# Performance work log

Measured on AMD Instinct MI355X. Metric: run time of the kernel, lower is better.

## Reference

```python
import jax, jax.numpy as jnp
import numpy as np
from jax.scipy.linalg import solve_triangular

B, D, O, K, R, HID = 8192, 64, 32, 15, 3, 60
LOG_2PI = float(np.log(2.0 * np.pi))


def setup_inputs() -> dict:
    key = jax.random.key(0)
    ks = jax.random.split(key, 12)
    state_mean = jax.random.normal(ks[0], (B, D), jnp.float32)
    A = jax.random.normal(ks[1], (B, D, D), jnp.float32) * 0.1
    state_cov = jnp.einsum('bik,bjk->bij', A, A) / D + 0.5 * jnp.eye(D, dtype=jnp.float32)
    obs = jax.random.normal(ks[2], (B, O), jnp.float32)
    w1 = jax.random.normal(ks[3], (HID, D), jnp.float32) / np.sqrt(D)
    b1 = jnp.zeros((HID,), jnp.float32)
    w2 = jax.random.normal(ks[4], (K, HID), jnp.float32) / np.sqrt(HID)
    b2 = jnp.zeros((K,), jnp.float32)
    basis = jax.random.normal(ks[5], (K, D, D), jnp.float32) * 0.01
    pnf = jax.random.normal(ks[6], (D, R), jnp.float32) * 0.1
    pnd = jnp.ones((D,), jnp.float32) * 0.1
    onf = jax.random.normal(ks[7], (O, R), jnp.float32) * 0.1
    ond = jnp.ones((O,), jnp.float32) * 0.1
    Hw = jax.random.normal(ks[8], (O, D), jnp.float32) / np.sqrt(D)
    Hb = jnp.zeros((O,), jnp.float32)
    return dict(state_mean=state_mean, state_cov=state_cov, obs=obs,
                w1=w1, b1=b1, w2=w2, b2=b2, basis=basis,
                pnf=pnf, pnd=pnd, onf=onf, ond=ond, Hw=Hw, Hb=Hb)


def _rkn_cell(state_mean, state_cov, obs, w1, b1, w2, b2, basis, pnf, pnd, onf, ond, Hw, Hb):
    # ---- predict step: locally linear dynamics ----
    h = jax.nn.elu(state_mean @ w1.T + b1)
    weights = jax.nn.softmax(h @ w2.T + b2, axis=-1)          # [B, K]
    F = jnp.einsum('bn,nij->bij', weights, basis)             # [B, D, D]
    pred_mean = jnp.einsum('bij,bj->bi', F, state_mean)
    FPFT = jnp.einsum('bij,bjk,blk->bil', F, state_cov, F)
    Q = pnf @ pnf.T + jnp.diag(jnp.exp(pnd))                  # [D, D] process noise
    pred_cov = FPFT + Q[None]

    # ---- update step ----
    obs_pred = pred_mean @ Hw.T + Hb
    innovation = obs - obs_pred                               # [B, O]
    HPH = jnp.einsum('oi,bij,pj->bop', Hw, pred_cov, Hw)      # [B, O, O]
    Rn = onf @ onf.T + jnp.diag(jnp.exp(ond))                 # [O, O] obs noise
    S = HPH + Rn[None]                                        # innovation cov
    PHt = jnp.einsum('bij,oj->bio', pred_cov, Hw)             # [B, D, O]

    L = jnp.linalg.cholesky(S)                                # [B, O, O]
    eyeO = jnp.broadcast_to(jnp.eye(O, dtype=S.dtype), (S.shape[0], O, O))
    Linv = solve_triangular(L, eyeO, lower=True)              # L^{-1}
    S_inv = jnp.einsum('bko,bkp->bop', Linv, Linv)            # cholesky_inverse

    Kg = jnp.einsum('bio,bop->bip', PHt, S_inv)               # Kalman gain [B, D, O]
    post_mean = pred_mean + jnp.einsum('bio,bo->bi', Kg, innovation)
    KH = jnp.einsum('bio,oj->bij', Kg, Hw)
    post_cov = jnp.einsum('bij,bjk->bik', jnp.eye(D, dtype=KH.dtype)[None] - KH, pred_cov)

    log_det = 2.0 * jnp.sum(jnp.log(jnp.diagonal(L, axis1=-2, axis2=-1)), axis=-1)
    quad = jnp.einsum('bo,bop,bp->b', innovation, S_inv, innovation)
    log_likelihood = -0.5 * (log_det + quad + O * LOG_2PI)
    return post_mean, post_cov, log_likelihood


def reference(state_mean, state_cov, obs, w1, b1, w2, b2, basis, pnf, pnd, onf, ond, Hw, Hb):
    return _rkn_cell(state_mean, state_cov, obs, w1, b1, w2, b2, basis, pnf, pnd, onf, ond, Hw, Hb)
```

## Files before the change

### kernel.cpp

```cpp
#include <hip/hip_runtime.h>
#include <math.h>

#define NB   8192
#define DD   64
#define OO   32
#define KK   15
#define HID  60

#define LDF  68
#define LDT  72
#define SST  36
#define XOFF (32*LDF)

#define LOG2PI 1.8378770664093453f

__global__ __launch_bounds__(256, 2)
void rkn_kernel(const float* __restrict__ state_mean,
                const float* __restrict__ state_cov,
                const float* __restrict__ obs,
                const float* __restrict__ w1,
                const float* __restrict__ b1,
                const float* __restrict__ w2,
                const float* __restrict__ b2,
                const float* __restrict__ basis,
                const float* __restrict__ pnf,
                const float* __restrict__ pnd,
                const float* __restrict__ onf,
                const float* __restrict__ ond,
                const float* __restrict__ Hw,
                const float* __restrict__ Hb,
                float* __restrict__ out_pm,
                float* __restrict__ out_pc,
                float* __restrict__ out_ll)
{
  __shared__ __align__(16) float sF [64*LDF];
  __shared__ __align__(16) float sP [64*LDF];
  __shared__ __align__(16) float sT [64*LDT];
  __shared__ __align__(16) float sHw[32*LDF];
  __shared__ __align__(16) float sS [32*SST];
  __shared__ __align__(16) float sm_[64];
  __shared__ __align__(16) float pm_[64];
  __shared__ __align__(16) float h_ [64];
  __shared__ __align__(16) float inn_[32];
  __shared__ __align__(16) float y_ [32];
  __shared__ float wts_[16];
  __shared__ float redA[32];
  __shared__ float rdiag_[32];
  __shared__ float qd_;
  __shared__ __align__(16) float spnf[64*4];
  __shared__ float spd[64];
  __shared__ __align__(16) float sonf[32*4];
  __shared__ float sod[32];

  const int t = threadIdx.x;
  const int b = blockIdx.x;

  {
    const float4* cov4 = (const float4*)(state_cov + (size_t)b * 4096);
    #pragma unroll
    for (int r = 0; r < 4; r++) {
      int idx = t + 256*r;
      int row = idx >> 4, c4 = idx & 15;
      *(float4*)&sP[row*LDF + c4*4] = cov4[idx];
    }
    const float4* hw4 = (const float4*)Hw;
    #pragma unroll
    for (int r = 0; r < 2; r++) {
      int idx = t + 256*r;
      int row = idx >> 4, c4 = idx & 15;
      *(float4*)&sHw[row*LDF + c4*4] = hw4[idx];
    }
    if (t < 64) {
      sm_[t] = state_mean[(size_t)b*64 + t];
      spnf[t*4+0] = pnf[t*3+0];
      spnf[t*4+1] = pnf[t*3+1];
      spnf[t*4+2] = pnf[t*3+2];
      spnf[t*4+3] = 0.0f;
      spd[t] = expf(pnd[t]);
    }
    if (t < 32) {
      sonf[t*4+0] = onf[t*3+0];
      sonf[t*4+1] = onf[t*3+1];
      sonf[t*4+2] = onf[t*3+2];
      sonf[t*4+3] = 0.0f;
      sod[t] = expf(ond[t]);
    }
  }
  __syncthreads();

  if (t < HID) {
    const float4* w1r = (const float4*)(w1 + t*64);
    float acc = 0.0f;
    #pragma unroll
    for (int m = 0; m < 16; m++) {
      float4 wv = w1r[m];
      float4 sv = *(const float4*)&sm_[4*m];
      acc += wv.x*sv.x + wv.y*sv.y + wv.z*sv.z + wv.w*sv.w;
    }
    acc += b1[t];
    h_[t] = (acc > 0.0f) ? acc : expm1f(acc);
  }
  __syncthreads();

  if (t < KK) {
    const float* w2r = w2 + t*60;
    float acc = 0.0f;
    for (int m = 0; m < 60; m++) acc += w2r[m]*h_[m];
    wts_[t] = acc + b2[t];
  }
  __syncthreads();

  if (t == 0) {
    float mx = wts_[0];
    for (int k = 1; k < KK; k++) mx = fmaxf(mx, wts_[k]);
    float s = 0.0f;
    for (int k = 0; k < KK; k++) { float e = expf(wts_[k]-mx); wts_[k] = e; s += e; }
    float inv = 1.0f/s;
    for (int k = 0; k < KK; k++) wts_[k] *= inv;
  }
  __syncthreads();

  {
    float w[KK];
    #pragma unroll
    for (int k = 0; k < KK; k++) w[k] = wts_[k];
    const float4* bas4 = (const float4*)basis;
    #pragma unroll
    for (int r = 0; r < 4; r++) {
      int idx = t + 256*r;
      float4 acc; acc.x = 0; acc.y = 0; acc.z = 0; acc.w = 0;
      #pragma unroll
      for (int k = 0; k < KK; k++) {
        float4 bv = bas4[k*1024 + idx];
        acc.x += w[k]*bv.x; acc.y += w[k]*bv.y;
        acc.z += w[k]*bv.z; acc.w += w[k]*bv.w;
      }
      int row = idx >> 4, c4 = idx & 15;
      *(float4*)&sF[row*LDF + c4*4] = acc;
    }
  }
  __syncthreads();

  const int tr = t >> 4, tc = t & 15;
  const int i0 = tr*4, j0 = tc*4;

  {
    float acc[4][4] = {};
    for (int k = 0; k < 64; k += 4) {
      float4 a[4], bb[4];
      #pragma unroll
      for (int r = 0; r < 4; r++) a[r] = *(const float4*)&sF[(i0+r)*LDF + k];
      #pragma unroll
      for (int kk = 0; kk < 4; kk++) bb[kk] = *(const float4*)&sP[(k+kk)*LDF + j0];
      #pragma unroll
      for (int r = 0; r < 4; r++) {
        float4 av = a[r];
        acc[r][0] += av.x*bb[0].x + av.y*bb[1].x + av.z*bb[2].x + av.w*bb[3].x;
        acc[r][1] += av.x*bb[0].y + av.y*bb[1].y + av.z*bb[2].y + av.w*bb[3].y;
        acc[r][2] += av.x*bb[0].z + av.y*bb[1].z + av.z*bb[2].z + av.w*bb[3].z;
        acc[r][3] += av.x*bb[0].w + av.y*bb[1].w + av.z*bb[2].w + av.w*bb[3].w;
      }
    }
    #pragma unroll
    for (int r = 0; r < 4; r++) {
      float4 st; st.x = acc[r][0]; st.y = acc[r][1]; st.z = acc[r][2]; st.w = acc[r][3];
      *(float4*)&sT[(i0+r)*LDT + j0] = st;
    }
  }
  if (t < 64) {
    float acc = 0.0f;
    #pragma unroll
    for (int m = 0; m < 16; m++) {
      float4 fv = *(const float4*)&sF[t*LDF + 4*m];
      float4 sv = *(const float4*)&sm_[4*m];
      acc += fv.x*sv.x + fv.y*sv.y + fv.z*sv.z + fv.w*sv.w;
    }
    pm_[t] = acc;
  }
  __syncthreads();

  {
    float acc[4][4] = {};
    for (int k = 0; k < 64; k += 4) {
      float4 a[4], bb[4];
      #pragma unroll
      for (int r = 0; r < 4; r++) a[r] = *(const float4*)&sT[(i0+r)*LDT + k];
      #pragma unroll
      for (int c = 0; c < 4; c++) bb[c] = *(const float4*)&sF[(j0+c)*LDF + k];
      #pragma unroll
      for (int r = 0; r < 4; r++) {
        #pragma unroll
        for (int c = 0; c < 4; c++) {
          acc[r][c] += a[r].x*bb[c].x + a[r].y*bb[c].y + a[r].z*bb[c].z + a[r].w*bb[c].w;
        }
      }
    }
    #pragma unroll
    for (int r = 0; r < 4; r++) {
      int i = i0 + r;
      float4 st;
      float* pst = (float*)&st;
      #pragma unroll
      for (int c = 0; c < 4; c++) {
        int j = j0 + c;
        float q = spnf[i*4+0]*spnf[j*4+0] + spnf[i*4+1]*spnf[j*4+1] + spnf[i*4+2]*spnf[j*4+2];
        if (i == j) q += spd[i];
        pst[c] = acc[r][c] + q;
      }
      *(float4*)&sP[i*LDF + j0] = st;
    }
  }
  if (t < 32) {
    float acc = 0.0f;
    #pragma unroll
    for (int m = 0; m < 16; m++) {
      float4 hv = *(const float4*)&sHw[t*LDF + 4*m];
      float4 pv = *(const float4*)&pm_[4*m];
      acc += hv.x*pv.x + hv.y*pv.y + hv.z*pv.z + hv.w*pv.w;
    }
    inn_[t] = obs[(size_t)b*32 + t] - (acc + Hb[t]);
  }
  __syncthreads();

  {
    const int hr0 = (t >> 4)*2, hc0 = (t & 15)*4;
    float acc[2][4] = {};
    for (int k = 0; k < 64; k += 4) {
      float4 a0 = *(const float4*)&sHw[hr0*LDF + k];
      float4 a1 = *(const float4*)&sHw[(hr0+1)*LDF + k];
      float4 bb[4];
      #pragma unroll
      for (int kk = 0; kk < 4; kk++) bb[kk] = *(const float4*)&sP[(k+kk)*LDF + hc0];
      #pragma unroll
      for (int c = 0; c < 4; c++) {
        float* pb0 = (float*)&bb[0]; float* pb1 = (float*)&bb[1];
        float* pb2 = (float*)&bb[2]; float* pb3 = (float*)&bb[3];
        acc[0][c] += a0.x*pb0[c] + a0.y*pb1[c] + a0.z*pb2[c] + a0.w*pb3[c];
        acc[1][c] += a1.x*pb0[c] + a1.y*pb1[c] + a1.z*pb2[c] + a1.w*pb3[c];
      }
    }
    float4 s0, s1;
    s0.x = acc[0][0]; s0.y = acc[0][1]; s0.z = acc[0][2]; s0.w = acc[0][3];
    s1.x = acc[1][0]; s1.y = acc[1][1]; s1.z = acc[1][2]; s1.w = acc[1][3];
    *(float4*)&sT[hr0*LDF + hc0] = s0;
    *(float4*)&sT[(hr0+1)*LDF + hc0] = s1;
  }
  __syncthreads();

  const int so = t >> 3, sp0 = (t & 7)*4;

  {
    float acc[4] = {};
    for (int k = 0; k < 64; k += 4) {
      float4 av = *(const float4*)&sT[so*LDF + k];
      #pragma unroll
      for (int c = 0; c < 4; c++) {
        float4 bv = *(const float4*)&sHw[(sp0+c)*LDF + k];
        acc[c] += av.x*bv.x + av.y*bv.y + av.z*bv.z + av.w*bv.w;
      }
    }
    #pragma unroll
    for (int c = 0; c < 4; c++) {
      int p = sp0 + c;
      float rn = sonf[so*4+0]*sonf[p*4+0] + sonf[so*4+1]*sonf[p*4+1] + sonf[so*4+2]*sonf[p*4+2];
      if (so == p) rn += sod[so];
      sS[so*SST + p] = acc[c] + rn;
    }
  }
  __syncthreads();

  for (int k = 0; k < 32; k++) {
    float dk  = sS[k*SST + k];
    float cik = sS[so*SST + k];
    float cj[4];
    #pragma unroll
    for (int c = 0; c < 4; c++) cj[c] = sS[(sp0+c)*SST + k];
    __syncthreads();
    float rd = 1.0f/dk;
    #pragma unroll
    for (int c = 0; c < 4; c++) {
      int j = sp0 + c;
      if (so > k && j > k) sS[so*SST + j] -= cik*cj[c]*rd;
    }
    if (k >= sp0 && k < sp0+4) {
      float sd = sqrtf(dk);
      if (so > k)       sS[so*SST + k] = cik/sd;
      else if (so == k) sS[k*SST + k]  = sd;
    }
    __syncthreads();
  }

  if (t < 32) {
    float d = sS[t*SST + t];
    rdiag_[t] = 1.0f/d;
    redA[t]  = logf(d);
  }
  __syncthreads();

  if (t < 65) {
    float x[32];
    if (t < 64) {
      #pragma unroll
      for (int i = 0; i < 32; i++) x[i] = sT[i*LDF + t];
    } else {
      #pragma unroll
      for (int i = 0; i < 32; i++) x[i] = inn_[i];
    }
    #pragma unroll
    for (int m = 0; m < 32; m++) {
      x[m] *= rdiag_[m];
      #pragma unroll
      for (int i = m+1; i < 32; i++) x[i] -= sS[i*SST + m] * x[m];
    }
    if (t < 64) {
      #pragma unroll
      for (int i = 0; i < 32; i++) sT[XOFF + i*LDF + t] = x[i];
    } else {
      float q = 0.0f;
      #pragma unroll
      for (int i = 0; i < 32; i++) { y_[i] = x[i]; q += x[i]*x[i]; }
      qd_ = q;
    }
  }
  __syncthreads();

  {
    float acc[4][4] = {};
    for (int o = 0; o < 32; o += 2) {
      float4 xa0 = *(const float4*)&sT[XOFF + o*LDF + i0];
      float4 xb0 = *(const float4*)&sT[XOFF + o*LDF + j0];
      float4 xa1 = *(const float4*)&sT[XOFF + (o+1)*LDF + i0];
      float4 xb1 = *(const float4*)&sT[XOFF + (o+1)*LDF + j0];
      const float* a0 = (const float*)&xa0; const float* b0 = (const float*)&xb0;
      const float* a1 = (const float*)&xa1; const float* b1p = (const float*)&xb1;
      #pragma unroll
      for (int r = 0; r < 4; r++) {
        #pragma unroll
        for (int c = 0; c < 4; c++) {
          acc[r][c] += a0[r]*b0[c] + a1[r]*b1p[c];
        }
      }
    }
    #pragma unroll
    for (int r = 0; r < 4; r++) {
      int i = i0 + r;
      float4 st;
      st.x = sP[i*LDF + j0+0] - acc[r][0];
      st.y = sP[i*LDF + j0+1] - acc[r][1];
      st.z = sP[i*LDF + j0+2] - acc[r][2];
      st.w = sP[i*LDF + j0+3] - acc[r][3];
      *(float4*)&out_pc[(size_t)b*4096 + i*64 + j0] = st;
    }
  }
  if (t < 64) {
    float acc = pm_[t];
    #pragma unroll
    for (int i = 0; i < 32; i++) acc += sT[XOFF + i*LDF + t] * y_[i];
    out_pm[(size_t)b*64 + t] = acc;
  }
  if (t == 0) {
    float ld = 0.0f;
    for (int k = 0; k < 32; k++) ld += redA[k];
    out_ll[b] = -0.5f*(2.0f*ld + qd_ + 32.0f*LOG2PI);
  }
}

extern "C" void kernel_launch(void* const* d_in, const int* in_sizes, int n_in,
                              void* d_out, int out_size, void* d_ws, size_t ws_size,
                              hipStream_t stream) {
  const float* state_mean = (const float*)d_in[0];
  const float* state_cov  = (const float*)d_in[1];
  const float* obs        = (const float*)d_in[2];
  const float* w1         = (const float*)d_in[3];
  const float* b1         = (const float*)d_in[4];
  const float* w2         = (const float*)d_in[5];
  const float* b2         = (const float*)d_in[6];
  const float* basis      = (const float*)d_in[7];
  const float* pnf        = (const float*)d_in[8];
  const float* pnd        = (const float*)d_in[9];
  const float* onf        = (const float*)d_in[10];
  const float* ond        = (const float*)d_in[11];
  const float* Hw         = (const float*)d_in[12];
  const float* Hb         = (const float*)d_in[13];

  const int Bn = in_sizes[0] / 64;
  float* out = (float*)d_out;
  float* out_pm = out;
  float* out_pc = out + (size_t)Bn*64;
  float* out_ll = out + (size_t)Bn*64 + (size_t)Bn*4096;

  hipLaunchKernelGGL(rkn_kernel, dim3(Bn), dim3(256), 0, stream,
                     state_mean, state_cov, obs, w1, b1, w2, b2, basis,
                     pnf, pnd, onf, ond, Hw, Hb, out_pm, out_pc, out_ll);
}
```

Measured before the change: 2.736 ms.

## Double block size, shrink per-thread tiles, warp-level Cholesky via shuffles

```diff
diff --git a/kernel.cpp b/kernel.cpp
--- a/kernel.cpp
+++ b/kernel.cpp
@@ -14,7 +14,9 @@
 
 #define LOG2PI 1.8378770664093453f
 
-__global__ __launch_bounds__(256, 2)
+typedef float f32x4 __attribute__((ext_vector_type(4)));
+
+__global__ __launch_bounds__(512, 4)
 void rkn_kernel(const float* __restrict__ state_mean,
                 const float* __restrict__ state_cov,
                 const float* __restrict__ obs,
@@ -58,17 +60,15 @@
   {
     const float4* cov4 = (const float4*)(state_cov + (size_t)b * 4096);
     #pragma unroll
-    for (int r = 0; r < 4; r++) {
-      int idx = t + 256*r;
+    for (int r = 0; r < 2; r++) {
+      int idx = t + 512*r;
       int row = idx >> 4, c4 = idx & 15;
       *(float4*)&sP[row*LDF + c4*4] = cov4[idx];
     }
     const float4* hw4 = (const float4*)Hw;
-    #pragma unroll
-    for (int r = 0; r < 2; r++) {
-      int idx = t + 256*r;
-      int row = idx >> 4, c4 = idx & 15;
-      *(float4*)&sHw[row*LDF + c4*4] = hw4[idx];
+    {
+      int row = t >> 4, c4 = t & 15;
+      *(float4*)&sHw[row*LDF + c4*4] = hw4[t];
     }
     if (t < 64) {
       sm_[t] = state_mean[(size_t)b*64 + t];
@@ -126,8 +126,8 @@
     for (int k = 0; k < KK; k++) w[k] = wts_[k];
     const float4* bas4 = (const float4*)basis;
     #pragma unroll
-    for (int r = 0; r < 4; r++) {
-      int idx = t + 256*r;
+    for (int r = 0; r < 2; r++) {
+      int idx = t + 512*r;
       float4 acc; acc.x = 0; acc.y = 0; acc.z = 0; acc.w = 0;
       #pragma unroll
       for (int k = 0; k < KK; k++) {
@@ -142,27 +142,26 @@
   __syncthreads();
 
   const int tr = t >> 4, tc = t & 15;
-  const int i0 = tr*4, j0 = tc*4;
-
-  {
-    float acc[4][4] = {};
+  const int i0 = tr*2, j0 = tc*4;
+
+  {
+    float acc[2][4] = {};
     for (int k = 0; k < 64; k += 4) {
-      float4 a[4], bb[4];
-      #pragma unroll
-      for (int r = 0; r < 4; r++) a[r] = *(const float4*)&sF[(i0+r)*LDF + k];
+      float4 a0 = *(const float4*)&sF[(i0  )*LDF + k];
+      float4 a1 = *(const float4*)&sF[(i0+1)*LDF + k];
+      float4 bb[4];
       #pragma unroll
       for (int kk = 0; kk < 4; kk++) bb[kk] = *(const float4*)&sP[(k+kk)*LDF + j0];
-      #pragma unroll
-      for (int r = 0; r < 4; r++) {
-        float4 av = a[r];
-        acc[r][0] += av.x*bb[0].x + av.y*bb[1].x + av.z*bb[2].x + av.w*bb[3].x;
-        acc[r][1] += av.x*bb[0].y + av.y*bb[1].y + av.z*bb[2].y + av.w*bb[3].y;
-        acc[r][2] += av.x*bb[0].z + av.y*bb[1].z + av.z*bb[2].z + av.w*bb[3].z;
-        acc[r][3] += av.x*bb[0].w + av.y*bb[1].w + av.z*bb[2].w + av.w*bb[3].w;
-      }
-    }
-    #pragma unroll
-    for (int r = 0; r < 4; r++) {
+      const float* b0 = (const float*)&bb[0]; const float* b1p = (const float*)&bb[1];
+      const float* b2p = (const float*)&bb[2]; const float* b3 = (const float*)&bb[3];
+      #pragma unroll
+      for (int c = 0; c < 4; c++) {
+        acc[0][c] += a0.x*b0[c] + a0.y*b1p[c] + a0.z*b2p[c] + a0.w*b3[c];
+        acc[1][c] += a1.x*b0[c] + a1.y*b1p[c] + a1.z*b2p[c] + a1.w*b3[c];
+      }
+    }
+    #pragma unroll
+    for (int r = 0; r < 2; r++) {
       float4 st; st.x = acc[r][0]; st.y = acc[r][1]; st.z = acc[r][2]; st.w = acc[r][3];
       *(float4*)&sT[(i0+r)*LDT + j0] = st;
     }
@@ -180,23 +179,19 @@
   __syncthreads();
 
   {
-    float acc[4][4] = {};
+    float acc[2][4] = {};
     for (int k = 0; k < 64; k += 4) {
-      float4 a[4], bb[4];
-      #pragma unroll
-      for (int r = 0; r < 4; r++) a[r] = *(const float4*)&sT[(i0+r)*LDT + k];
-      #pragma unroll
-      for (int c = 0; c < 4; c++) bb[c] = *(const float4*)&sF[(j0+c)*LDF + k];
-      #pragma unroll
-      for (int r = 0; r < 4; r++) {
-        #pragma unroll
-        for (int c = 0; c < 4; c++) {
-          acc[r][c] += a[r].x*bb[c].x + a[r].y*bb[c].y + a[r].z*bb[c].z + a[r].w*bb[c].w;
-        }
-      }
-    }
-    #pragma unroll
-    for (int r = 0; r < 4; r++) {
+      float4 a0 = *(const float4*)&sT[(i0  )*LDT + k];
+      float4 a1 = *(const float4*)&sT[(i0+1)*LDT + k];
+      #pragma unroll
+      for (int c = 0; c < 4; c++) {
+        float4 bv = *(const float4*)&sF[(j0+c)*LDF + k];
+        acc[0][c] += a0.x*bv.x + a0.y*bv.y + a0.z*bv.z + a0.w*bv.w;
+        acc[1][c] += a1.x*bv.x + a1.y*bv.y + a1.z*bv.z + a1.w*bv.w;
+      }
+    }
+    #pragma unroll
+    for (int r = 0; r < 2; r++) {
       int i = i0 + r;
       float4 st;
       float* pst = (float*)&st;
@@ -223,33 +218,26 @@
   __syncthreads();
 
   {
-    const int hr0 = (t >> 4)*2, hc0 = (t & 15)*4;
-    float acc[2][4] = {};
+    const int hr = t >> 4, hc0 = (t & 15)*4;
+    float acc[4] = {};
     for (int k = 0; k < 64; k += 4) {
-      float4 a0 = *(const float4*)&sHw[hr0*LDF + k];
-      float4 a1 = *(const float4*)&sHw[(hr0+1)*LDF + k];
+      float4 a = *(const float4*)&sHw[hr*LDF + k];
       float4 bb[4];
       #pragma unroll
       for (int kk = 0; kk < 4; kk++) bb[kk] = *(const float4*)&sP[(k+kk)*LDF + hc0];
-      #pragma unroll
-      for (int c = 0; c < 4; c++) {
-        float* pb0 = (float*)&bb[0]; float* pb1 = (float*)&bb[1];
-        float* pb2 = (float*)&bb[2]; float* pb3 = (float*)&bb[3];
-        acc[0][c] += a0.x*pb0[c] + a0.y*pb1[c] + a0.z*pb2[c] + a0.w*pb3[c];
-        acc[1][c] += a1.x*pb0[c] + a1.y*pb1[c] + a1.z*pb2[c] + a1.w*pb3[c];
-      }
-    }
-    float4 s0, s1;
-    s0.x = acc[0][0]; s0.y = acc[0][1]; s0.z = acc[0][2]; s0.w = acc[0][3];
-    s1.x = acc[1][0]; s1.y = acc[1][1]; s1.z = acc[1][2]; s1.w = acc[1][3];
-    *(float4*)&sT[hr0*LDF + hc0] = s0;
-    *(float4*)&sT[(hr0+1)*LDF + hc0] = s1;
-  }
-  __syncthreads();
-
-  const int so = t >> 3, sp0 = (t & 7)*4;
-
-  {
+      const float* b0 = (const float*)&bb[0]; const float* b1p = (const float*)&bb[1];
+      const float* b2p = (const float*)&bb[2]; const float* b3 = (const float*)&bb[3];
+      #pragma unroll
+      for (int c = 0; c < 4; c++)
+        acc[c] += a.x*b0[c] + a.y*b1p[c] + a.z*b2p[c] + a.w*b3[c];
+    }
+    float4 s0; s0.x = acc[0]; s0.y = acc[1]; s0.z = acc[2]; s0.w = acc[3];
+    *(float4*)&sT[hr*LDF + hc0] = s0;
+  }
+  __syncthreads();
+
+  if (t < 256) {
+    const int so = t >> 3, sp0 = (t & 7)*4;
     float acc[4] = {};
     for (int k = 0; k < 64; k += 4) {
       float4 av = *(const float4*)&sT[so*LDF + k];
@@ -269,35 +257,36 @@
   }
   __syncthreads();
 
-  for (int k = 0; k < 32; k++) {
-    float dk  = sS[k*SST + k];
-    float cik = sS[so*SST + k];
-    float cj[4];
-    #pragma unroll
-    for (int c = 0; c < 4; c++) cj[c] = sS[(sp0+c)*SST + k];
-    __syncthreads();
-    float rd = 1.0f/dk;
-    #pragma unroll
-    for (int c = 0; c < 4; c++) {
-      int j = sp0 + c;
-      if (so > k && j > k) sS[so*SST + j] -= cik*cj[c]*rd;
-    }
-    if (k >= sp0 && k < sp0+4) {
+  if (t < 64) {
+    const int lane = t;
+    const int li = (lane < 32) ? lane : 0;
+    float r[32];
+    #pragma unroll
+    for (int j = 0; j < 32; j++) r[j] = sS[li*SST + j];
+    float my_sd = 1.0f;
+    #pragma unroll
+    for (int k = 0; k < 32; k++) {
+      float dk = __shfl(r[k], k);
       float sd = sqrtf(dk);
-      if (so > k)       sS[so*SST + k] = cik/sd;
-      else if (so == k) sS[k*SST + k]  = sd;
-    }
-    __syncthreads();
-  }
-
-  if (t < 32) {
-    float d = sS[t*SST + t];
-    rdiag_[t] = 1.0f/d;
-    redA[t]  = logf(d);
-  }
-  __syncthreads();
-
-  if (t < 65) {
+      float lik = r[k] * (1.0f/sd);
+      if (lane == k) my_sd = sd;
+      r[k] = lik;
+      #pragma unroll
+      for (int j = k+1; j < 32; j++) {
+        float ljk = __shfl(lik, j);
+        if (lane >= j) r[j] -= lik * ljk;
+      }
+    }
+    if (lane < 32) {
+      #pragma unroll
+      for (int j = 0; j < 32; j++) sS[lane*SST + j] = r[j];
+      rdiag_[lane] = 1.0f / my_sd;
+      redA[lane]   = logf(my_sd);
+    }
+  }
+  __syncthreads();
+
+  if (t < 128) {
     float x[32];
     if (t < 64) {
       #pragma unroll
@@ -315,7 +304,7 @@
     if (t < 64) {
       #pragma unroll
       for (int i = 0; i < 32; i++) sT[XOFF + i*LDF + t] = x[i];
-    } else {
+    } else if (t == 64) {
       float q = 0.0f;
       #pragma unroll
       for (int i = 0; i < 32; i++) { y_[i] = x[i]; q += x[i]*x[i]; }
@@ -325,38 +314,33 @@
   __syncthreads();
 
   {
-    float acc[4][4] = {};
-    for (int o = 0; o < 32; o += 2) {
-      float4 xa0 = *(const float4*)&sT[XOFF + o*LDF + i0];
-      float4 xb0 = *(const float4*)&sT[XOFF + o*LDF + j0];
-      float4 xa1 = *(const float4*)&sT[XOFF + (o+1)*LDF + i0];
-      float4 xb1 = *(const float4*)&sT[XOFF + (o+1)*LDF + j0];
-      const float* a0 = (const float*)&xa0; const float* b0 = (const float*)&xb0;
-      const float* a1 = (const float*)&xa1; const float* b1p = (const float*)&xb1;
-      #pragma unroll
-      for (int r = 0; r < 4; r++) {
-        #pragma unroll
-        for (int c = 0; c < 4; c++) {
-          acc[r][c] += a0[r]*b0[c] + a1[r]*b1p[c];
-        }
-      }
-    }
-    #pragma unroll
-    for (int r = 0; r < 4; r++) {
+    float acc[2][4] = {};
+    for (int o = 0; o < 32; o++) {
+      float2 xa = *(const float2*)&sT[XOFF + o*LDF + i0];
+      float4 xb = *(const float4*)&sT[XOFF + o*LDF + j0];
+      const float* bp = (const float*)&xb;
+      #pragma unroll
+      for (int c = 0; c < 4; c++) {
+        acc[0][c] += xa.x * bp[c];
+        acc[1][c] += xa.y * bp[c];
+      }
+    }
+    #pragma unroll
+    for (int r = 0; r < 2; r++) {
       int i = i0 + r;
-      float4 st;
+      f32x4 st;
       st.x = sP[i*LDF + j0+0] - acc[r][0];
       st.y = sP[i*LDF + j0+1] - acc[r][1];
       st.z = sP[i*LDF + j0+2] - acc[r][2];
       st.w = sP[i*LDF + j0+3] - acc[r][3];
-      *(float4*)&out_pc[(size_t)b*4096 + i*64 + j0] = st;
+      __builtin_nontemporal_store(st, (f32x4*)&out_pc[(size_t)b*4096 + i*64 + j0]);
     }
   }
   if (t < 64) {
     float acc = pm_[t];
     #pragma unroll
     for (int i = 0; i < 32; i++) acc += sT[XOFF + i*LDF + t] * y_[i];
-    out_pm[(size_t)b*64 + t] = acc;
+    __builtin_nontemporal_store(acc, &out_pm[(size_t)b*64 + t]);
   }
   if (t == 0) {
     float ld = 0.0f;
@@ -389,7 +373,7 @@
   float* out_pc = out + (size_t)Bn*64;
   float* out_ll = out + (size_t)Bn*64 + (size_t)Bn*4096;
 
-  hipLaunchKernelGGL(rkn_kernel, dim3(Bn), dim3(256), 0, stream,
+  hipLaunchKernelGGL(rkn_kernel, dim3(Bn), dim3(512), 0, stream,
                      state_mean, state_cov, obs, w1, b1, w2, b2, basis,
                      pnf, pnd, onf, ond, Hw, Hb, out_pm, out_pc, out_ll);
 }
```

After: 3.956 ms. 1.45x slower.
